# Kernel optimization log

Measured on AMD Instinct MI355X. Metric: run time of the kernel, lower is better.

Reference implementation:

```python
import jax, jax.numpy as jnp
import numpy as np

L = 8       # num decoder layers
S = 192     # seq_len = h*w = 24*8
D = 512     # d_model
DFF = 2048  # dim_feedforward
H, W, BS = 24, 8, 16
EPS = 1e-5


def setup_inputs() -> dict:
    key = jax.random.key(0)
    ks = jax.random.split(key, 8)
    f = jax.random.normal
    return {
        "q_feat": f(ks[0], (BS, D * L, H, W), jnp.float32),
        "g_feat": f(ks[1], (BS, D * L, H, W), jnp.float32),
        "targets": jax.random.randint(ks[2], (BS,), 0, 8),
        "score_embed": f(ks[3], (L, S, S), jnp.float32) * 0.05,
        "fc0_w": f(ks[4], (L, D, D), jnp.float32) * (1.0 / np.sqrt(D)),
        "fc0_b": jnp.zeros((L, D), jnp.float32),
        "bn1_g": jnp.ones((L,), jnp.float32),
        "bn1_b": jnp.zeros((L,), jnp.float32),
        "fc2_w": f(ks[5], (L, DFF, S), jnp.float32) * (1.0 / np.sqrt(S)),
        "fc2_b": jnp.zeros((L, DFF), jnp.float32),
        "bn2_g": jnp.ones((L, DFF), jnp.float32),
        "bn2_b": jnp.zeros((L, DFF), jnp.float32),
        "fc3_w": f(ks[6], (L, DFF), jnp.float32) * (1.0 / np.sqrt(DFF)),
        "fc3_b": jnp.zeros((L,), jnp.float32),
        "bn3_g": jnp.ones((L,), jnp.float32),
        "bn3_b": jnp.zeros((L,), jnp.float32),
    }


def _layer(qf, gf, se, w0, b0, g1, b1, w2, b2, g2, bb2, w3, b3, g3, bb3):
    # qf: [q,s,d], gf: [k,s,d]; shared fc0 projection for query and key
    query = jnp.einsum('qsd,ed->qse', qf, w0) + b0
    key_ = jnp.einsum('ksd,ed->kse', gf, w0) + b0
    # 4D correlation volume masked by sigmoid of learned score embedding
    score = jnp.einsum('qtd,ksd->qkst', query, key_) * jax.nn.sigmoid(se)
    q, k = score.shape[0], score.shape[1]
    sc = score.reshape(q * k, S, S)
    cat = jnp.concatenate([sc.max(axis=1), sc.max(axis=2)], axis=-1)  # [qk, 2S]
    x = cat.reshape(-1, S)  # [2qk, S]  (matches torch view(-1,1,S))
    # bn1: single channel -> normalize over all elements (training-mode BN)
    x = g1 * (x - x.mean()) * jax.lax.rsqrt(x.var() + EPS) + b1
    x = x @ w2.T + b2  # [2qk, DFF]
    mu = x.mean(0)
    var = x.var(0)
    x = g2 * (x - mu) * jax.lax.rsqrt(var + EPS) + bb2
    x = jax.nn.relu(x)
    x = x @ w3 + b3  # [2qk]
    x = x.reshape(-1, 2).sum(-1)  # [qk]: sum of row-max branch and col-max branch
    x = g3 * (x - x.mean()) * jax.lax.rsqrt(x.var() + EPS) + bb3
    return x.reshape(q, k)


def reference(q_feat, g_feat, targets, score_embed, fc0_w, fc0_b, bn1_g, bn1_b,
              fc2_w, fc2_b, bn2_g, bn2_b, fc3_w, fc3_b, bn3_g, bn3_b):
    bs = q_feat.shape[0]
    qf = jnp.transpose(q_feat, (0, 2, 3, 1)).reshape(bs, S, D * L)
    gf = jnp.transpose(g_feat, (0, 2, 3, 1)).reshape(bs, S, D * L)
    score = None
    for i in range(L):  # fixed small layer loop; each layer has distinct params
        si = _layer(qf[..., i * D:(i + 1) * D], gf[..., i * D:(i + 1) * D],
                    score_embed[i], fc0_w[i], fc0_b[i], bn1_g[i], bn1_b[i],
                    fc2_w[i], fc2_b[i], bn2_g[i], bn2_b[i],
                    fc3_w[i], fc3_b[i], bn3_g[i], bn3_b[i])
        score = si if score is None else score + si
    pair_labels = (targets[:, None] == targets[None, :]).astype(jnp.float32)
    return score, pair_labels
```

## Files before the change

### kernel.cpp

```cpp
#include <hip/hip_runtime.h>
#include <hip/hip_bf16.h>


#define EPS_ 1e-5f

typedef __attribute__((ext_vector_type(8))) _Float16 fp16x8;
typedef __attribute__((ext_vector_type(4)))  float   f32x4;
typedef __attribute__((ext_vector_type(16))) float   f32x16;

__device__ __forceinline__ unsigned fkey(float f) {
    unsigned u = __float_as_uint(f);
    return (u & 0x80000000u) ? ~u : (u | 0x80000000u);
}
__device__ __forceinline__ float funkey(unsigned k) {
    return (k & 0x80000000u) ? __uint_as_float(k & 0x7FFFFFFFu)
                             : __uint_as_float(~k);
}
__device__ __forceinline__ void gld16(const void* gp, void* lp) {
    __builtin_amdgcn_global_load_lds(
        (const __attribute__((address_space(1))) unsigned*)gp,
        (__attribute__((address_space(3))) unsigned*)lp, 16, 0, 0);
}

__global__ __launch_bounds__(256) void k_prep(const float* __restrict__ se,
                                              float* __restrict__ sig,
                                              const float* __restrict__ w2,
                                              _Float16* __restrict__ w2h,
                                              unsigned* __restrict__ xkey,
                                              float* __restrict__ bn2z) {
    int b = blockIdx.x;
    int tid = threadIdx.x;
    if (b < 3072) {
        int i = b * 256 + tid;
        float4 v = *(const float4*)(w2 + (size_t)i * 4);
        _Float16 h[4] = {(_Float16)v.x, (_Float16)v.y, (_Float16)v.z, (_Float16)v.w};
        *(uint2*)(w2h + (size_t)i * 4) = *(uint2*)h;
    } else if (b < 3360) {
        int i = (b - 3072) * 256 + tid;
        float4 v = *(const float4*)(se + (size_t)i * 4);
        float4 o;
        o.x = 1.f / (1.f + __expf(-v.x));
        o.y = 1.f / (1.f + __expf(-v.y));
        o.z = 1.f / (1.f + __expf(-v.z));
        o.w = 1.f / (1.f + __expf(-v.w));
        *(float4*)(sig + (size_t)i * 4) = o;
    } else if (b < 3552) {
        int i = (b - 3360) * 256 + tid;
        uint4 z = {0u, 0u, 0u, 0u};
        uint4* p = (uint4*)xkey + (size_t)i * 4;
        p[0] = z; p[1] = z; p[2] = z; p[3] = z;
    } else {
        int i = (b - 3552) * 256 + tid;
        if (i < 8196) {
            float4 z = {0.f, 0.f, 0.f, 0.f};
            *(float4*)(bn2z + (size_t)i * 4) = z;
        }
    }
}

__global__ __launch_bounds__(256) void k_fc0(const float* __restrict__ qfeat,
                                             const float* __restrict__ gfeat,
                                             const float* __restrict__ w0,
                                             const float* __restrict__ b0,
                                             _Float16* __restrict__ Qh) {
    int bid = blockIdx.x;
    int et = bid & 1;  bid >>= 1;
    int tt = bid % 3;  bid /= 3;
    int b  = bid & 15; bid >>= 4;
    int l  = bid & 7;  bid >>= 3;
    int sel = bid;
    const float* feat  = sel ? gfeat : qfeat;
    const float* Af = feat + (size_t)b * 4096 * 192 + (size_t)l * 512 * 192;
    const float* Wf = w0 + (size_t)l * 262144;
    int t0 = tt * 64, e0 = et * 256;

    __shared__ __align__(16) char At[64 * 80];
    __shared__ __align__(16) char Bt[256 * 80];

    int tid = threadIdx.x;
    int lane = tid & 63;
    int w = tid >> 6;
    int half = lane >> 5;
    int lrow = lane & 31;

    f32x16 acc[2][2];
    #pragma unroll
    for (int mi = 0; mi < 2; mi++)
        #pragma unroll
        for (int ni = 0; ni < 2; ni++)
            #pragma unroll
            for (int r = 0; r < 16; r++) acc[mi][ni][r] = 0.f;

    for (int d0 = 0; d0 < 512; d0 += 32) {
        __syncthreads();
        {
            int tA = tid & 63;
            int dp = tid >> 6;
            #pragma unroll
            for (int r = 0; r < 4; r++) {
                int d = dp * 2 + r * 8;
                float v0 = Af[(size_t)(d0 + d) * 192 + t0 + tA];
                float v1 = Af[(size_t)(d0 + d + 1) * 192 + t0 + tA];
                _Float16 h2[2] = {(_Float16)v0, (_Float16)v1};
                *(unsigned*)(At + tA * 80 + d * 2) = *(unsigned*)h2;
            }
        }
        {
            #pragma unroll
            for (int p = 0; p < 8; p++) {
                int s = tid + p * 256;
                int e = s >> 3;
                int q = s & 7;
                float4 wv = *(const float4*)(Wf + (size_t)(e0 + e) * 512 + d0 + q * 4);
                _Float16 h[4] = {(_Float16)wv.x, (_Float16)wv.y, (_Float16)wv.z, (_Float16)wv.w};
                *(uint2*)(Bt + e * 80 + q * 8) = *(uint2*)h;
            }
        }
        __syncthreads();
        #pragma unroll
        for (int ks = 0; ks < 2; ks++) {
            int koff = ks * 32 + half * 16;
            fp16x8 a[2], bf[2];
            #pragma unroll
            for (int mi = 0; mi < 2; mi++)
                a[mi] = *(const fp16x8*)(At + (mi * 32 + lrow) * 80 + koff);
            #pragma unroll
            for (int ni = 0; ni < 2; ni++)
                bf[ni] = *(const fp16x8*)(Bt + (w * 64 + ni * 32 + lrow) * 80 + koff);
            #pragma unroll
            for (int mi = 0; mi < 2; mi++)
                #pragma unroll
                for (int ni = 0; ni < 2; ni++)
                    acc[mi][ni] = __builtin_amdgcn_mfma_f32_32x32x16_f16(a[mi], bf[ni], acc[mi][ni], 0, 0, 0);
        }
    }

    _Float16* Obase = Qh + ((size_t)(sel * 8 + l) * 16 + b) * 98304;
    #pragma unroll
    for (int ni = 0; ni < 2; ni++) {
        int e = e0 + w * 64 + ni * 32 + lrow;
        float bias = b0[l * 512 + e];
        #pragma unroll
        for (int mi = 0; mi < 2; mi++) {
            #pragma unroll
            for (int r = 0; r < 16; r++) {
                int t = t0 + mi * 32 + (r & 3) + 8 * (r >> 2) + 4 * half;
                Obase[(size_t)t * 512 + e] = (_Float16)(acc[mi][ni][r] + bias);
            }
        }
    }
}

#define BARP() do { __builtin_amdgcn_s_barrier(); \
                    __builtin_amdgcn_sched_barrier(0); } while (0)

__global__ __launch_bounds__(512, 2) void k_score(const _Float16* __restrict__ Qh,
                                                  const float* __restrict__ sig,
                                                  unsigned* __restrict__ xkey,
                                                  int base) {
    int bid = blockIdx.x + base;
    int l = bid & 7;
    int tau = bid >> 3;
    int mt = tau % 12;
    int nt = tau / 12;
    int m0 = mt * 256, n0 = nt * 256;

    const char* Ag = (const char*)(Qh + (size_t)(8 + l) * 1572864);
    const char* Bg = (const char*)(Qh + (size_t)l * 1572864);

    __shared__ __align__(16) char smem[131072];

    int tid = threadIdx.x;
    int lane = tid & 63;
    int w = tid >> 6;
    int wm = w >> 2, wn = w & 3;
    int c = lane & 15;
    int hi4 = lane >> 4;

    int pk0 = ((hi4)     ^ (c & 7)) * 16;
    int pk1 = ((4 + hi4) ^ (c & 7)) * 16;
    char* aBase = smem + wm * 16384 + c * 128;
    char* bBase = smem + 65536 + (wn >> 1) * 16384 + ((wn & 1) * 64 + c) * 128;

    int rl = lane >> 3;
    int qsw = ((lane & 7) ^ rl) * 16;
    const char* Asrc = Ag + (size_t)(m0 + w * 8 + rl) * 1024 + qsw;
    const char* Bsrc = Bg + (size_t)(n0 + w * 8 + rl) * 1024 + qsw;
    char* aSt = smem + w * 1024;
    char* bSt = smem + 65536 + w * 1024;

    f32x4 acc[8][4];
    #pragma unroll
    for (int mi = 0; mi < 8; mi++)
        #pragma unroll
        for (int nj = 0; nj < 4; nj++)
            #pragma unroll
            for (int r = 0; r < 4; r++) acc[mi][nj][r] = 0.f;

    fp16x8 a[4][2], b01[2][2], b23[2][2];

    auto STA = [&](int t, int h) {
        if (t < 8) {
            const char* s = Asrc + (size_t)(h * 128) * 1024 + t * 128;
            char* d = aSt + (t & 1) * 32768 + h * 16384;
            gld16(s, d);
            gld16(s + 64 * 1024, d + 8192);
        }
    };
    auto STB = [&](int t, int h) {
        if (t < 8) {
            const char* s = Bsrc + (size_t)(h * 128) * 1024 + t * 128;
            char* d = bSt + (t & 1) * 32768 + h * 16384;
            gld16(s, d);
            gld16(s + 64 * 1024, d + 8192);
        }
    };
    auto LDA = [&](int t, int mh) {
        const char* p = aBase + (t & 1) * 32768 + mh * 8192;
        #pragma unroll
        for (int m = 0; m < 4; m++) {
            a[m][0] = *(const fp16x8*)(p + m * 2048 + pk0);
            a[m][1] = *(const fp16x8*)(p + m * 2048 + pk1);
        }
    };
    auto LDB = [&](int t, int nh, fp16x8 (&bb)[2][2]) {
        const char* p = bBase + (t & 1) * 32768 + nh * 4096;
        #pragma unroll
        for (int n = 0; n < 2; n++) {
            bb[n][0] = *(const fp16x8*)(p + n * 2048 + pk0);
            bb[n][1] = *(const fp16x8*)(p + n * 2048 + pk1);
        }
    };
    auto MM = [&](int mh, int nh, fp16x8 (&bb)[2][2]) {
        #pragma unroll
        for (int ks = 0; ks < 2; ks++)
            #pragma unroll
            for (int m = 0; m < 4; m++)
                #pragma unroll
                for (int n = 0; n < 2; n++)
                    acc[mh * 4 + m][nh * 2 + n] = __builtin_amdgcn_mfma_f32_16x16x32_f16(
                        a[m][ks], bb[n][ks], acc[mh * 4 + m][nh * 2 + n], 0, 0, 0);
    };

    STB(0, 0); STB(0, 1); STA(0, 0); STA(0, 1); STB(1, 0); STB(1, 1);
    asm volatile("s_waitcnt vmcnt(4)");
    BARP();

    #pragma unroll
    for (int it = 0; it < 4; it++) {
        int T = 2 * it, U = 2 * it + 1;
        LDA(T, 0); LDB(T, 0, b01); STA(U, 0); BARP();
        __builtin_amdgcn_s_setprio(1); MM(0, 0, b01); __builtin_amdgcn_s_setprio(0); BARP();
        LDB(T, 1, b23); STA(U, 1); BARP();
        __builtin_amdgcn_s_setprio(1); MM(0, 1, b23); __builtin_amdgcn_s_setprio(0); BARP();
        LDA(T, 1); STB(T + 2, 0); BARP();
        __builtin_amdgcn_s_setprio(1); MM(1, 0, b01); __builtin_amdgcn_s_setprio(0); BARP();
        STB(T + 2, 1); BARP();
        __builtin_amdgcn_s_setprio(1); MM(1, 1, b23); __builtin_amdgcn_s_setprio(0);
        if (it < 3) { asm volatile("s_waitcnt vmcnt(4)"); }
        else        { asm volatile("s_waitcnt vmcnt(0)"); }
        BARP();
        LDA(U, 0); LDB(U, 0, b01); STA(T + 2, 0); BARP();
        __builtin_amdgcn_s_setprio(1); MM(0, 0, b01); __builtin_amdgcn_s_setprio(0); BARP();
        LDB(U, 1, b23); STA(T + 2, 1); BARP();
        __builtin_amdgcn_s_setprio(1); MM(0, 1, b23); __builtin_amdgcn_s_setprio(0); BARP();
        LDA(U, 1); STB(T + 3, 0); BARP();
        __builtin_amdgcn_s_setprio(1); MM(1, 0, b01); __builtin_amdgcn_s_setprio(0); BARP();
        STB(T + 3, 1); BARP();
        __builtin_amdgcn_s_setprio(1); MM(1, 1, b23); __builtin_amdgcn_s_setprio(0);
        if (it < 3) { asm volatile("s_waitcnt vmcnt(4)"); }
        BARP();
    }

    __syncthreads();

    int rq = hi4 * 4;
    int gcb = n0 + wn * 64;
    int qq = gcb / 192;
    int tb = gcb - qq * 192;
    (void)qq;
    const float* sg = sig + (size_t)l * 36864;

    float rowm[8][4];
    float colm[2][4];
    #pragma unroll
    for (int mi = 0; mi < 8; mi++)
        #pragma unroll
        for (int r = 0; r < 4; r++) rowm[mi][r] = -3.4e38f;
    #pragma unroll
    for (int h = 0; h < 2; h++)
        #pragma unroll
        for (int nj = 0; nj < 4; nj++) colm[h][nj] = -3.4e38f;

    #pragma unroll
    for (int mi = 0; mi < 8; mi++) {
        int gm = m0 + wm * 128 + mi * 16;
        int sb = gm % 192;
        #pragma unroll
        for (int r = 0; r < 4; r++) {
            const float* sp = sg + (size_t)(sb + rq + r) * 192 + tb;
            #pragma unroll
            for (int nj = 0; nj < 4; nj++) {
                float v = acc[mi][nj][r] * sp[nj * 16 + c];
                rowm[mi][r] = fmaxf(rowm[mi][r], v);
                colm[mi >> 2][nj] = fmaxf(colm[mi >> 2][nj], v);
            }
        }
    }
    #pragma unroll
    for (int st = 1; st <= 8; st <<= 1)
        #pragma unroll
        for (int mi = 0; mi < 8; mi++)
            #pragma unroll
            for (int r = 0; r < 4; r++)
                rowm[mi][r] = fmaxf(rowm[mi][r], __shfl_xor(rowm[mi][r], st));
    #pragma unroll
    for (int h = 0; h < 2; h++)
        #pragma unroll
        for (int nj = 0; nj < 4; nj++) {
            colm[h][nj] = fmaxf(colm[h][nj], __shfl_xor(colm[h][nj], 16));
            colm[h][nj] = fmaxf(colm[h][nj], __shfl_xor(colm[h][nj], 32));
        }

    unsigned* red = (unsigned*)smem;
    if (c == 0) {
        #pragma unroll
        for (int mi = 0; mi < 8; mi++)
            #pragma unroll
            for (int r = 0; r < 4; r++)
                red[w * 256 + mi * 16 + rq + r] = fkey(rowm[mi][r]);
    }
    if (lane < 16) {
        #pragma unroll
        for (int h = 0; h < 2; h++)
            #pragma unroll
            for (int nj = 0; nj < 4; nj++)
                red[w * 256 + 128 + h * 64 + nj * 16 + lane] = fkey(colm[h][nj]);
    }
    __syncthreads();
    #pragma unroll
    for (int pass = 0; pass < 4; pass++) {
        int flat = pass * 512 + tid;
        unsigned val = red[flat];
        int ww = flat >> 8;
        int rem = flat & 255;
        int wmf = ww >> 2, wnf = ww & 3;
        int gcbf = n0 + wnf * 64;
        int qqf = gcbf / 192;
        size_t addr;
        if (rem < 128) {
            int gmf = m0 + wmf * 128 + rem;
            int kkf = gmf / 192;
            int sf = gmf - kkf * 192;
            addr = ((size_t)l * 512 + 2 * (qqf * 16 + kkf) + 1) * 192 + sf;
        } else {
            int ii = rem - 128;
            int hh = ii >> 6, cc = ii & 63;
            int kkf = (m0 + wmf * 128 + hh * 64) / 192;
            addr = ((size_t)l * 512 + 2 * (qqf * 16 + kkf)) * 192 + (gcbf - qqf * 192) + cc;
        }
        atomicMax(&xkey[addr], val);
    }
}

__global__ __launch_bounds__(256) void k_bn1s(const unsigned* __restrict__ xkey,
                                              float* __restrict__ bn1acc) {
    int l = blockIdx.x / 48;
    int b = blockIdx.x - l * 48;
    const unsigned* xk = xkey + (size_t)l * 98304 + b * 2048;
    int tid = threadIdx.x;
    uint4 v1 = *(const uint4*)(xk + tid * 8);
    uint4 v2 = *(const uint4*)(xk + tid * 8 + 4);
    float s = 0.f, s2 = 0.f;
    float e;
    e = funkey(v1.x); s += e; s2 += e * e;
    e = funkey(v1.y); s += e; s2 += e * e;
    e = funkey(v1.z); s += e; s2 += e * e;
    e = funkey(v1.w); s += e; s2 += e * e;
    e = funkey(v2.x); s += e; s2 += e * e;
    e = funkey(v2.y); s += e; s2 += e * e;
    e = funkey(v2.z); s += e; s2 += e * e;
    e = funkey(v2.w); s += e; s2 += e * e;
    #pragma unroll
    for (int o = 32; o; o >>= 1) { s += __shfl_down(s, o); s2 += __shfl_down(s2, o); }
    if ((tid & 63) == 0) {
        atomicAdd(&bn1acc[l * 2], s);
        atomicAdd(&bn1acc[l * 2 + 1], s2);
    }
}

__global__ __launch_bounds__(256) void k_bn1n(const unsigned* __restrict__ xkey,
                                              const float* __restrict__ bn1acc,
                                              const float* __restrict__ g1,
                                              const float* __restrict__ b1,
                                              _Float16* __restrict__ xh) {
    int idx = blockIdx.x * 256 + threadIdx.x;
    int l = idx / 24576;
    float mu = bn1acc[l * 2] * (1.f / 98304.f);
    float var = bn1acc[l * 2 + 1] * (1.f / 98304.f) - mu * mu;
    float a1 = g1[l] * rsqrtf(var + EPS_);
    float c1 = b1[l] - mu * a1;
    uint4 kv = *(const uint4*)(xkey + (size_t)idx * 4);
    _Float16 h[4];
    h[0] = (_Float16)(funkey(kv.x) * a1 + c1);
    h[1] = (_Float16)(funkey(kv.y) * a1 + c1);
    h[2] = (_Float16)(funkey(kv.z) * a1 + c1);
    h[3] = (_Float16)(funkey(kv.w) * a1 + c1);
    *(uint2*)(xh + (size_t)idx * 4) = *(uint2*)h;
}

__global__ __launch_bounds__(256) void k_fc2(const _Float16* __restrict__ xh,
                                             const _Float16* __restrict__ w2h,
                                             const float* __restrict__ b2,
                                             _Float16* __restrict__ hb,
                                             float* __restrict__ bn2sum,
                                             float* __restrict__ bn2sq) {
    int bid = blockIdx.x;
    int l = bid >> 6;
    int rem = bid & 63;
    int mt = rem & 3, nt = rem >> 2;
    int m0 = mt * 128, n0 = nt * 128;
    const char* Ag = (const char*)(xh + (size_t)l * 98304);
    const char* Bg = (const char*)(w2h + (size_t)l * 393216);

    __shared__ __align__(16) char As[8192];
    __shared__ __align__(16) char Bs[8192];

    int tid = threadIdx.x;
    int lane = tid & 63;
    int w = tid >> 6;
    int wm = w >> 1, wn = w & 1;

    f32x4 acc[4][4];
    #pragma unroll
    for (int mi = 0; mi < 4; mi++)
        #pragma unroll
        for (int nj = 0; nj < 4; nj++)
            #pragma unroll
            for (int r = 0; r < 4; r++) acc[mi][nj][r] = 0.f;

    int srow = lane >> 2;
    int sseg = ((lane & 3) ^ ((srow >> 1) & 3)) * 16;
    int c = lane & 15;
    int kqp = (((lane >> 4) ^ ((c >> 1) & 3))) * 16;

    for (int d0 = 0; d0 < 384; d0 += 64) {
        __syncthreads();
        #pragma unroll
        for (int j = 0; j < 2; j++) {
            int r = w * 32 + j * 16 + srow;
            gld16(Ag + (size_t)(m0 + r) * 384 + d0 + sseg, As + (w * 32 + j * 16) * 64);
            gld16(Bg + (size_t)(n0 + r) * 384 + d0 + sseg, Bs + (w * 32 + j * 16) * 64);
        }
        __syncthreads();
        fp16x8 a[4], b[4];
        #pragma unroll
        for (int mi = 0; mi < 4; mi++)
            a[mi] = *(const fp16x8*)(As + (wm * 64 + mi * 16 + c) * 64 + kqp);
        #pragma unroll
        for (int nj = 0; nj < 4; nj++)
            b[nj] = *(const fp16x8*)(Bs + (wn * 64 + nj * 16 + c) * 64 + kqp);
        #pragma unroll
        for (int mi = 0; mi < 4; mi++)
            #pragma unroll
            for (int nj = 0; nj < 4; nj++)
                acc[mi][nj] = __builtin_amdgcn_mfma_f32_16x16x32_f16(a[mi], b[nj], acc[mi][nj], 0, 0, 0);
    }

    int rq = (lane >> 4) * 4;
    _Float16* ho = hb + (size_t)l * 1048576;
    float colsum[4], colsq[4];
    #pragma unroll
    for (int nj = 0; nj < 4; nj++) { colsum[nj] = 0.f; colsq[nj] = 0.f; }
    #pragma unroll
    for (int nj = 0; nj < 4; nj++) {
        int gf = n0 + wn * 64 + nj * 16 + c;
        float bias = b2[l * 2048 + gf];
        #pragma unroll
        for (int mi = 0; mi < 4; mi++) {
            #pragma unroll
            for (int r = 0; r < 4; r++) {
                int gm = m0 + wm * 64 + mi * 16 + rq + r;
                float v = acc[mi][nj][r] + bias;
                ho[(size_t)gm * 2048 + gf] = (_Float16)v;
                colsum[nj] += v;
                colsq[nj] += v * v;
            }
        }
    }
    #pragma unroll
    for (int nj = 0; nj < 4; nj++) {
        colsum[nj] += __shfl_xor(colsum[nj], 16);
        colsum[nj] += __shfl_xor(colsum[nj], 32);
        colsq[nj]  += __shfl_xor(colsq[nj], 16);
        colsq[nj]  += __shfl_xor(colsq[nj], 32);
    }
    if (lane < 16) {
        #pragma unroll
        for (int nj = 0; nj < 4; nj++) {
            int gf = n0 + wn * 64 + nj * 16 + lane;
            atomicAdd(&bn2sum[l * 2048 + gf], colsum[nj]);
            atomicAdd(&bn2sq[l * 2048 + gf], colsq[nj]);
        }
    }
}

__global__ __launch_bounds__(256) void k_coef(const float* __restrict__ bn2sum,
                                              const float* __restrict__ bn2sq,
                                              const float* __restrict__ g2,
                                              const float* __restrict__ bb2,
                                              float* __restrict__ coef) {
    int i = blockIdx.x * 256 + threadIdx.x;
    float mu = bn2sum[i] * (1.f / 512.f);
    float var = bn2sq[i] * (1.f / 512.f) - mu * mu;
    float a2 = g2[i] * rsqrtf(var + EPS_);
    coef[i] = a2;
    coef[16384 + i] = bb2[i] - mu * a2;
}

__global__ __launch_bounds__(256) void k_fc3(const _Float16* __restrict__ hb,
                                             const float* __restrict__ coef,
                                             const float* __restrict__ w3,
                                             const float* __restrict__ b3,
                                             float* __restrict__ ybuf) {
    int n = blockIdx.x & 511;
    int l = blockIdx.x >> 9;
    const _Float16* h = hb + ((size_t)l * 512 + n) * 2048;
    int tid = threadIdx.x;
    int f0 = tid * 8;
    fp16x8 hv = *(const fp16x8*)(h + f0);
    const float* cA = coef + l * 2048 + f0;
    const float* cC = coef + 16384 + l * 2048 + f0;
    const float* w3p = w3 + l * 2048 + f0;
    float4 a0 = *(const float4*)(cA), a1 = *(const float4*)(cA + 4);
    float4 c0 = *(const float4*)(cC), c1 = *(const float4*)(cC + 4);
    float4 w0 = *(const float4*)(w3p), w1 = *(const float4*)(w3p + 4);
    float sum = 0.f;
    float va[8] = {a0.x, a0.y, a0.z, a0.w, a1.x, a1.y, a1.z, a1.w};
    float vc[8] = {c0.x, c0.y, c0.z, c0.w, c1.x, c1.y, c1.z, c1.w};
    float vw[8] = {w0.x, w0.y, w0.z, w0.w, w1.x, w1.y, w1.z, w1.w};
    #pragma unroll
    for (int j = 0; j < 8; j++) {
        float v = (float)hv[j] * va[j] + vc[j];
        v = fmaxf(v, 0.f);
        sum += v * vw[j];
    }
    __shared__ float red[4];
    int lane = tid & 63, w = tid >> 6;
    #pragma unroll
    for (int o = 32; o; o >>= 1) sum += __shfl_down(sum, o);
    if (lane == 0) red[w] = sum;
    __syncthreads();
    if (tid == 0) ybuf[l * 512 + n] = red[0] + red[1] + red[2] + red[3] + b3[l];
}

__global__ __launch_bounds__(256) void k_final(const float* __restrict__ ybuf,
                                               const float* __restrict__ g3,
                                               const float* __restrict__ bb3,
                                               const int* __restrict__ targets,
                                               float* __restrict__ out) {
    int tid = threadIdx.x;
    __shared__ float red[8];
    float scoreacc = 0.f;
    for (int l = 0; l < 8; l++) {
        float z = ybuf[l * 512 + 2 * tid] + ybuf[l * 512 + 2 * tid + 1];
        float s = z, s2 = z * z;
        int lane = tid & 63, w = tid >> 6;
        #pragma unroll
        for (int o = 32; o; o >>= 1) { s += __shfl_down(s, o); s2 += __shfl_down(s2, o); }
        if (lane == 0) { red[w] = s; red[4 + w] = s2; }
        __syncthreads();
        float S1 = red[0] + red[1] + red[2] + red[3];
        float S2 = red[4] + red[5] + red[6] + red[7];
        float mu = S1 * (1.f / 256.f);
        float var = S2 * (1.f / 256.f) - mu * mu;
        float rstd = rsqrtf(var + EPS_);
        scoreacc += g3[l] * (z - mu) * rstd + bb3[l];
        __syncthreads();
    }
    out[tid] = scoreacc;
    int i = tid >> 4, j = tid & 15;
    out[256 + tid] = (targets[i] == targets[j]) ? 1.f : 0.f;
}

extern "C" void kernel_launch(void* const* d_in, const int* in_sizes, int n_in,
                              void* d_out, int out_size, void* d_ws, size_t ws_size,
                              hipStream_t stream) {
    const float* q_feat = (const float*)d_in[0];
    const float* g_feat = (const float*)d_in[1];
    const int*   targets = (const int*)d_in[2];
    const float* se     = (const float*)d_in[3];
    const float* fc0_w  = (const float*)d_in[4];
    const float* fc0_b  = (const float*)d_in[5];
    const float* bn1_g  = (const float*)d_in[6];
    const float* bn1_b  = (const float*)d_in[7];
    const float* fc2_w  = (const float*)d_in[8];
    const float* fc2_b  = (const float*)d_in[9];
    const float* bn2_g  = (const float*)d_in[10];
    const float* bn2_b  = (const float*)d_in[11];
    const float* fc3_w  = (const float*)d_in[12];
    const float* fc3_b  = (const float*)d_in[13];
    const float* bn3_g  = (const float*)d_in[14];
    const float* bn3_b  = (const float*)d_in[15];

    float* ws = (float*)d_ws;
    _Float16* Qh   = (_Float16*)ws;
    float*    sig  = ws + 12582912;
    unsigned* xkey = (unsigned*)(ws + 12877824);
    _Float16* xh   = (_Float16*)(ws + 13664256);
    _Float16* w2h  = (_Float16*)(ws + 14057472);
    _Float16* hb   = (_Float16*)(ws + 15630336);
    float* bn2sum = ws + 19824640;
    float* bn2sq  = ws + 19841024;
    float* bn1acc = ws + 19857408;
    float* ybuf   = ws + 19857424;
    float* out  = (float*)d_out;

    k_prep<<<3585, 256, 0, stream>>>(se, sig, fc2_w, w2h, xkey, bn2sum);
    k_fc0<<<1536, 256, 0, stream>>>(q_feat, g_feat, fc0_w, fc0_b, Qh);
    k_score<<<256, 512, 0, stream>>>(Qh, sig, xkey, 0);
    k_score<<<256, 512, 0, stream>>>(Qh, sig, xkey, 256);
    k_score<<<256, 512, 0, stream>>>(Qh, sig, xkey, 512);
    k_score<<<256, 512, 0, stream>>>(Qh, sig, xkey, 768);
    k_score<<<128, 512, 0, stream>>>(Qh, sig, xkey, 1024);
    k_bn1s<<<384, 256, 0, stream>>>(xkey, bn1acc);
    k_bn1n<<<768, 256, 0, stream>>>(xkey, bn1acc, bn1_g, bn1_b, xh);
    k_fc2<<<512, 256, 0, stream>>>(xh, w2h, fc2_b, hb, bn2sum, bn2sq);
    k_coef<<<64, 256, 0, stream>>>(bn2sum, bn2sq, bn2_g, bn2_b, sig);
    k_fc3<<<4096, 256, 0, stream>>>(hb, sig, fc3_w, fc3_b, ybuf);
    k_final<<<1, 256, 0, stream>>>(ybuf, bn3_g, bn3_b, targets, out);
}
```

Measured before the change: 410.0 us.

## Pre-convert fc0 weights to swizzled fp16 and retile fc0 GEMM with double buffering

Adds a kernel that converts fc0 weights once to fp16 in an XOR-swizzled layout inside the workspace, aliased with the later hb buffer. The fc0 GEMM is rewritten with 512-thread blocks covering the full 192-row sequence by 256 output columns, 16x16x32 MFMAs, and double-buffered LDS. Activations are prefetched into registers and weights are loaded asynchronously with global_load_lds. This cuts redundant weight conversion and global traffic across row tiles and overlaps loads with compute, at the cost of an extra launch and heavy LDS and register use.

```diff
diff --git a/kernel.cpp b/kernel.cpp
--- a/kernel.cpp
+++ b/kernel.cpp
@@ -58,95 +58,155 @@
     }
 }
 
-__global__ __launch_bounds__(256) void k_fc0(const float* __restrict__ qfeat,
-                                             const float* __restrict__ gfeat,
-                                             const float* __restrict__ w0,
-                                             const float* __restrict__ b0,
-                                             _Float16* __restrict__ Qh) {
+__global__ __launch_bounds__(256) void k_cvt0(const float* __restrict__ w0,
+                                              _Float16* __restrict__ w0h) {
+    int g = blockIdx.x * 256 + threadIdx.x;
+    int l  = g >> 15;
+    int r  = g & 32767;
+    int ks = r >> 12;
+    int rr = r & 4095;
+    int e  = rr >> 3;
+    int ch = rr & 7;
+    const float* src = w0 + (size_t)l * 262144 + (size_t)e * 512 + ks * 64 + ch * 8;
+    float4 v0 = *(const float4*)src;
+    float4 v1 = *(const float4*)(src + 4);
+    fp16x8 h;
+    h[0] = (_Float16)v0.x; h[1] = (_Float16)v0.y; h[2] = (_Float16)v0.z; h[3] = (_Float16)v0.w;
+    h[4] = (_Float16)v1.x; h[5] = (_Float16)v1.y; h[6] = (_Float16)v1.z; h[7] = (_Float16)v1.w;
+    size_t dst = ((size_t)(l * 8 + ks) * 512 + e) * 8 + (ch ^ (e & 7));
+    *(fp16x8*)(w0h + dst * 8) = h;
+}
+
+__global__ __launch_bounds__(512, 2) void k_fc0(const float* __restrict__ qfeat,
+                                                const float* __restrict__ gfeat,
+                                                const _Float16* __restrict__ w0h,
+                                                const float* __restrict__ b0,
+                                                _Float16* __restrict__ Qh) {
     int bid = blockIdx.x;
-    int et = bid & 1;  bid >>= 1;
-    int tt = bid % 3;  bid /= 3;
-    int b  = bid & 15; bid >>= 4;
-    int l  = bid & 7;  bid >>= 3;
-    int sel = bid;
-    const float* feat  = sel ? gfeat : qfeat;
-    const float* Af = feat + (size_t)b * 4096 * 192 + (size_t)l * 512 * 192;
-    const float* Wf = w0 + (size_t)l * 262144;
-    int t0 = tt * 64, e0 = et * 256;
-
-    __shared__ __align__(16) char At[64 * 80];
-    __shared__ __align__(16) char Bt[256 * 80];
+    int blo = bid & 7;
+    int et  = (bid >> 3) & 1;
+    int bhi = (bid >> 4) & 1;
+    int sel = (bid >> 5) & 1;
+    int l   = bid >> 6;
+    int b   = blo + bhi * 8;
+
+    const float* feat = sel ? gfeat : qfeat;
+    const float* Af = feat + (size_t)b * 786432 + (size_t)l * 98304;
+
+    __shared__ __align__(16) char smem[114688];
 
     int tid = threadIdx.x;
     int lane = tid & 63;
     int w = tid >> 6;
-    int half = lane >> 5;
-    int lrow = lane & 31;
-
-    f32x16 acc[2][2];
-    #pragma unroll
-    for (int mi = 0; mi < 2; mi++)
-        #pragma unroll
-        for (int ni = 0; ni < 2; ni++)
-            #pragma unroll
-            for (int r = 0; r < 16; r++) acc[mi][ni][r] = 0.f;
-
-    for (int d0 = 0; d0 < 512; d0 += 32) {
+    int wm = w >> 2, wn = w & 3;
+    int c = lane & 15;
+    int hi4 = lane >> 4;
+
+    int s0 = tid, s1 = tid + 512, s2 = tid + 1024;
+    int ch0 = s0 / 192, t0 = s0 - ch0 * 192;
+    int ch1 = s1 / 192, t1 = s1 - ch1 * 192;
+    int ch2 = s2 / 192, t2 = s2 - ch2 * 192;
+    const float* ap0 = Af + ch0 * 1536 + t0;
+    const float* ap1 = Af + ch1 * 1536 + t1;
+    const float* ap2 = Af + ch2 * 1536 + t2;
+    int aw0 = t0 * 128 + ((ch0 ^ (t0 & 7)) << 4);
+    int aw1 = t1 * 128 + ((ch1 ^ (t1 & 7)) << 4);
+    int aw2 = t2 * 128 + ((ch2 ^ (t2 & 7)) << 4);
+
+    f32x4 acc[6][4];
+    #pragma unroll
+    for (int mi = 0; mi < 6; mi++)
+        #pragma unroll
+        for (int nj = 0; nj < 4; nj++)
+            #pragma unroll
+            for (int r = 0; r < 4; r++) acc[mi][nj][r] = 0.f;
+
+    float rA[3][8];
+
+    auto ALOAD = [&](int ks) {
+        int off = ks * 12288;
+        #pragma unroll
+        for (int j = 0; j < 8; j++) rA[0][j] = ap0[off + j * 192];
+        #pragma unroll
+        for (int j = 0; j < 8; j++) rA[1][j] = ap1[off + j * 192];
+        #pragma unroll
+        for (int j = 0; j < 8; j++) rA[2][j] = ap2[off + j * 192];
+    };
+    auto WLOAD = [&](int ks, int buf) {
+        const _Float16* wp = w0h + ((size_t)(l * 8 + ks) * 512 + et * 256) * 64;
+        char* d = smem + 49152 + buf * 32768;
+        #pragma unroll
+        for (int p = 0; p < 4; p++)
+            gld16(wp + (size_t)(tid + p * 512) * 8, d + (tid + p * 512) * 16);
+    };
+    auto AWRITE = [&](int buf) {
+        char* db = smem + buf * 24576;
+        fp16x8 h0, h1, h2;
+        #pragma unroll
+        for (int j = 0; j < 8; j++) h0[j] = (_Float16)rA[0][j];
+        #pragma unroll
+        for (int j = 0; j < 8; j++) h1[j] = (_Float16)rA[1][j];
+        #pragma unroll
+        for (int j = 0; j < 8; j++) h2[j] = (_Float16)rA[2][j];
+        *(fp16x8*)(db + aw0) = h0;
+        *(fp16x8*)(db + aw1) = h1;
+        *(fp16x8*)(db + aw2) = h2;
+    };
+    auto COMPUTE = [&](int buf) {
+        const char* Ab = smem + buf * 24576;
+        const char* Wb = smem + 49152 + buf * 32768;
+        fp16x8 afr[6][2], bfr[4][2];
+        #pragma unroll
+        for (int mi = 0; mi < 6; mi++) {
+            int tr = wm * 96 + mi * 16 + c;
+            #pragma unroll
+            for (int k2 = 0; k2 < 2; k2++) {
+                int ph = (k2 * 4 + hi4) ^ (tr & 7);
+                afr[mi][k2] = *(const fp16x8*)(Ab + tr * 128 + ph * 16);
+            }
+        }
+        #pragma unroll
+        for (int nj = 0; nj < 4; nj++) {
+            int er = wn * 64 + nj * 16 + c;
+            #pragma unroll
+            for (int k2 = 0; k2 < 2; k2++) {
+                int ph = (k2 * 4 + hi4) ^ (er & 7);
+                bfr[nj][k2] = *(const fp16x8*)(Wb + er * 128 + ph * 16);
+            }
+        }
+        #pragma unroll
+        for (int k2 = 0; k2 < 2; k2++)
+            #pragma unroll
+            for (int mi = 0; mi < 6; mi++)
+                #pragma unroll
+                for (int nj = 0; nj < 4; nj++)
+                    acc[mi][nj] = __builtin_amdgcn_mfma_f32_16x16x32_f16(
+                        afr[mi][k2], bfr[nj][k2], acc[mi][nj], 0, 0, 0);
+    };
+
+    ALOAD(0); WLOAD(0, 0); AWRITE(0);
+    __syncthreads();
+    #pragma unroll
+    for (int ks = 0; ks < 8; ks++) {
+        int cur = ks & 1, nxt = cur ^ 1;
+        if (ks < 7) { ALOAD(ks + 1); WLOAD(ks + 1, nxt); }
+        COMPUTE(cur);
+        if (ks < 7) AWRITE(nxt);
         __syncthreads();
-        {
-            int tA = tid & 63;
-            int dp = tid >> 6;
-            #pragma unroll
-            for (int r = 0; r < 4; r++) {
-                int d = dp * 2 + r * 8;
-                float v0 = Af[(size_t)(d0 + d) * 192 + t0 + tA];
-                float v1 = Af[(size_t)(d0 + d + 1) * 192 + t0 + tA];
-                _Float16 h2[2] = {(_Float16)v0, (_Float16)v1};
-                *(unsigned*)(At + tA * 80 + d * 2) = *(unsigned*)h2;
-            }
-        }
-        {
-            #pragma unroll
-            for (int p = 0; p < 8; p++) {
-                int s = tid + p * 256;
-                int e = s >> 3;
-                int q = s & 7;
-                float4 wv = *(const float4*)(Wf + (size_t)(e0 + e) * 512 + d0 + q * 4);
-                _Float16 h[4] = {(_Float16)wv.x, (_Float16)wv.y, (_Float16)wv.z, (_Float16)wv.w};
-                *(uint2*)(Bt + e * 80 + q * 8) = *(uint2*)h;
-            }
-        }
-        __syncthreads();
-        #pragma unroll
-        for (int ks = 0; ks < 2; ks++) {
-            int koff = ks * 32 + half * 16;
-            fp16x8 a[2], bf[2];
-            #pragma unroll
-            for (int mi = 0; mi < 2; mi++)
-                a[mi] = *(const fp16x8*)(At + (mi * 32 + lrow) * 80 + koff);
-            #pragma unroll
-            for (int ni = 0; ni < 2; ni++)
-                bf[ni] = *(const fp16x8*)(Bt + (w * 64 + ni * 32 + lrow) * 80 + koff);
-            #pragma unroll
-            for (int mi = 0; mi < 2; mi++)
-                #pragma unroll
-                for (int ni = 0; ni < 2; ni++)
-                    acc[mi][ni] = __builtin_amdgcn_mfma_f32_32x32x16_f16(a[mi], bf[ni], acc[mi][ni], 0, 0, 0);
-        }
-    }
-
-    _Float16* Obase = Qh + ((size_t)(sel * 8 + l) * 16 + b) * 98304;
-    #pragma unroll
-    for (int ni = 0; ni < 2; ni++) {
-        int e = e0 + w * 64 + ni * 32 + lrow;
+    }
+
+    _Float16* Ob = Qh + ((size_t)(sel * 8 + l) * 16 + b) * 98304;
+    int rq = hi4 * 4;
+    #pragma unroll
+    for (int nj = 0; nj < 4; nj++) {
+        int e = et * 256 + wn * 64 + nj * 16 + c;
         float bias = b0[l * 512 + e];
         #pragma unroll
-        for (int mi = 0; mi < 2; mi++) {
-            #pragma unroll
-            for (int r = 0; r < 16; r++) {
-                int t = t0 + mi * 32 + (r & 3) + 8 * (r >> 2) + 4 * half;
-                Obase[(size_t)t * 512 + e] = (_Float16)(acc[mi][ni][r] + bias);
-            }
+        for (int mi = 0; mi < 6; mi++) {
+            int tb = wm * 96 + mi * 16 + rq;
+            #pragma unroll
+            for (int r = 0; r < 4; r++)
+                Ob[(size_t)(tb + r) * 512 + e] = (_Float16)(acc[mi][nj][r] + bias);
         }
     }
 }
@@ -610,6 +670,7 @@
     _Float16* xh   = (_Float16*)(ws + 13664256);
     _Float16* w2h  = (_Float16*)(ws + 14057472);
     _Float16* hb   = (_Float16*)(ws + 15630336);
+    _Float16* w0h  = (_Float16*)(ws + 15630336);
     float* bn2sum = ws + 19824640;
     float* bn2sq  = ws + 19841024;
     float* bn1acc = ws + 19857408;
@@ -617,7 +678,8 @@
     float* out  = (float*)d_out;
 
     k_prep<<<3585, 256, 0, stream>>>(se, sig, fc2_w, w2h, xkey, bn2sum);
-    k_fc0<<<1536, 256, 0, stream>>>(q_feat, g_feat, fc0_w, fc0_b, Qh);
+    k_cvt0<<<1024, 256, 0, stream>>>(fc0_w, w0h);
+    k_fc0<<<512, 512, 0, stream>>>(q_feat, g_feat, w0h, fc0_b, Qh);
     k_score<<<256, 512, 0, stream>>>(Qh, sig, xkey, 0);
     k_score<<<256, 512, 0, stream>>>(Qh, sig, xkey, 256);
     k_score<<<256, 512, 0, stream>>>(Qh, sig, xkey, 512);
```

After: 377.8 us. 7.9% less time.
